# Optimization experiments

Hardware: AMD Instinct MI355X
Metric: run time of the kernel (lower is better)

The kernel has to match this reference:

```python
import jax, jax.numpy as jnp
import numpy as np

D_MODEL, D_FF, N_EXPERTS, TOP_K = 1024, 2048, 8, 2
B, S = 2, 2048

def setup_inputs() -> dict:
    key = jax.random.key(0)
    k1, k2, k3, k4 = jax.random.split(key, 4)
    scale = 0.02
    return {
        "x": jax.random.normal(k1, (B, S, D_MODEL), dtype=jnp.float32),
        "gate_w": jax.random.normal(k2, (D_MODEL, N_EXPERTS), dtype=jnp.float32) * scale,
        "w1": jax.random.normal(k3, (N_EXPERTS, D_MODEL, D_FF), dtype=jnp.float32) * scale,
        "w2": jax.random.normal(k4, (N_EXPERTS, D_FF, D_MODEL), dtype=jnp.float32) * scale,
    }

def reference(x, gate_w, w1, w2):
    # --- Router (eval mode: no exploration noise, no dropout) ---
    router_logits = jnp.einsum('bsd,de->bse', x, gate_w)          # [B,S,E]
    top_logits, top_idx = jax.lax.top_k(router_logits, TOP_K)      # [B,S,K]
    top_w = jax.nn.softmax(top_logits, axis=-1)                    # [B,S,K]
    # topk indices are distinct per token, so per-(token,expert) combine weight
    # is the sum over k of weight_k * 1[idx_k == e] (matches torch gather/argmax logic)
    combine = jnp.sum(
        jax.nn.one_hot(top_idx, N_EXPERTS, dtype=x.dtype) * top_w[..., None],
        axis=-2)                                                   # [B,S,E]
    # --- Experts: dense-compute formulation of the gather/MLP/scatter loop ---
    h = jax.nn.silu(jnp.einsum('bsd,edf->ebsf', x, w1))            # [E,B,S,Dff]
    y = jnp.einsum('ebsf,efd->ebsd', h, w2)                        # [E,B,S,D]
    out = jnp.einsum('ebsd,bse->bsd', y, combine)                  # [B,S,D]
    return out
```

## Files before the change

### kernel.cpp

```cpp
#include <hip/hip_runtime.h>
#include <cstdint>
#include <cstddef>

#define D_MODEL 1024
#define D_FF    2048
#define N_EXP   8
#define NTOK    4096
#define NASSIGN (NTOK * 2)
#define MAXTILE 72

typedef __bf16 bf16_t;
typedef bf16_t bf16x8 __attribute__((ext_vector_type(8)));
typedef float  f32x4  __attribute__((ext_vector_type(4)));

typedef __attribute__((address_space(3))) void       lds_void;
typedef const __attribute__((address_space(1))) void gl_void;

__device__ __forceinline__ unsigned short f2b(float f) {
  union { float f; unsigned u; } v; v.f = f;
  unsigned u = v.u;
  unsigned r = (u + 0x7FFFu + ((u >> 16) & 1u)) >> 16;
  return (unsigned short)r;
}
__device__ __forceinline__ float b2f(unsigned short b) {
  union { unsigned u; float f; } v; v.u = ((unsigned)b) << 16; return v.f;
}

__device__ __forceinline__ void transpose_strip4(
    const float* __restrict__ ein, unsigned short* __restrict__ eout,
    int R, int C, int c00, int r0, unsigned* T0, unsigned* T1, int tid)
{
  const int g = tid >> 4;
  const int m = tid & 15;
  const int sh = (g & 1) * 16;

  float4 v[4][4];
  #pragma unroll
  for (int t = 0; t < 4; ++t)
    #pragma unroll
    for (int i = 0; i < 4; ++i)
      v[t][i] = *(const float4*)(ein + (size_t)(r0 + i * 16 + g) * C + (c00 + t * 64) + m * 4);

  #define PACK(BUF, VT)                                                      \
    _Pragma("unroll")                                                        \
    for (int i = 0; i < 4; ++i) {                                            \
      unsigned lo = (unsigned)f2b(VT[i].x) | ((unsigned)f2b(VT[i].y) << 16); \
      unsigned hi = (unsigned)f2b(VT[i].z) | ((unsigned)f2b(VT[i].w) << 16); \
      unsigned* p = (BUF) + (i * 16 + g) * 33 + m * 2;                       \
      p[0] = lo; p[1] = hi;                                                  \
    }
  #define STORE(BUF, T)                                                      \
    _Pragma("unroll")                                                        \
    for (int i = 0; i < 4; ++i) {                                            \
      int c = i * 16 + g;                                                    \
      ushort4 o;                                                             \
      o.x = (unsigned short)((BUF)[(4 * m + 0) * 33 + (c >> 1)] >> sh);      \
      o.y = (unsigned short)((BUF)[(4 * m + 1) * 33 + (c >> 1)] >> sh);      \
      o.z = (unsigned short)((BUF)[(4 * m + 2) * 33 + (c >> 1)] >> sh);      \
      o.w = (unsigned short)((BUF)[(4 * m + 3) * 33 + (c >> 1)] >> sh);      \
      *(ushort4*)(eout + (size_t)(c00 + (T) * 64 + c) * R + r0 + m * 4) = o; \
    }

  PACK(T0, v[0]);
  __syncthreads();
  STORE(T0, 0); PACK(T1, v[1]);
  __syncthreads();
  STORE(T1, 1); PACK(T0, v[2]);
  __syncthreads();
  STORE(T0, 2); PACK(T1, v[3]);
  __syncthreads();
  STORE(T1, 3);
  #undef PACK
  #undef STORE
}

__global__ __launch_bounds__(256) void prep_k(
    const float* __restrict__ x, const float* __restrict__ gw,
    const float* __restrict__ w1, const float* __restrict__ w2,
    unsigned short* __restrict__ w1t, unsigned short* __restrict__ w2t,
    int* __restrict__ eidx, float* __restrict__ ewt)
{
  __shared__ unsigned T[2][64 * 33];
  const int bid = blockIdx.x;
  const int tid = threadIdx.x;

  if (bid < 1024) {
    int e = bid >> 7, rem = bid & 127;
    int bs = rem & 7, by = rem >> 3;
    transpose_strip4(w1 + (size_t)e * D_MODEL * D_FF,
                     w1t + (size_t)e * D_MODEL * D_FF,
                     D_MODEL, D_FF, bs * 256, by * 64, T[0], T[1], tid);
    return;
  }
  if (bid < 2048) {
    int b = bid - 1024;
    int e = b >> 7, rem = b & 127;
    int bs = rem & 3, by = rem >> 2;
    transpose_strip4(w2 + (size_t)e * D_MODEL * D_FF,
                     w2t + (size_t)e * D_MODEL * D_FF,
                     D_FF, D_MODEL, bs * 256, by * 64, T[0], T[1], tid);
    return;
  }
  const int rb = bid - 2048;
  const int wv = tid >> 6, lane = tid & 63;
  const int token = rb * 4 + wv;
  const float4* xr4 = (const float4*)(x + (size_t)token * D_MODEL);
  const float4* gw4 = (const float4*)gw;

  float acc[8] = {};
  #pragma unroll
  for (int it = 0; it < 4; ++it) {
    float4 xv = xr4[it * 64 + lane];
    int d0 = it * 256 + lane * 4;
    #pragma unroll
    for (int i = 0; i < 4; ++i) {
      int d = d0 + i;
      float4 g0 = gw4[d * 2];
      float4 g1 = gw4[d * 2 + 1];
      float xs = (i == 0) ? xv.x : (i == 1) ? xv.y : (i == 2) ? xv.z : xv.w;
      acc[0] += xs * g0.x; acc[1] += xs * g0.y;
      acc[2] += xs * g0.z; acc[3] += xs * g0.w;
      acc[4] += xs * g1.x; acc[5] += xs * g1.y;
      acc[6] += xs * g1.z; acc[7] += xs * g1.w;
    }
  }
  #pragma unroll
  for (int m = 1; m < 64; m <<= 1) {
    #pragma unroll
    for (int k = 0; k < 8; ++k) acc[k] += __shfl_xor(acc[k], m);
  }
  if (lane == 0) {
    int i1 = 0; float v1 = acc[0];
    #pragma unroll
    for (int k = 1; k < 8; ++k) if (acc[k] > v1) { v1 = acc[k]; i1 = k; }
    int i2 = -1; float v2 = -1e30f;
    #pragma unroll
    for (int k = 0; k < 8; ++k) if (k != i1 && acc[k] > v2) { v2 = acc[k]; i2 = k; }
    float t  = __expf(v2 - v1);
    float wa = 1.f / (1.f + t);
    float wb = t * wa;
    eidx[token * 2 + 0] = i1; eidx[token * 2 + 1] = i2;
    ewt [token * 2 + 0] = wa; ewt [token * 2 + 1] = wb;
  }
}

__global__ __launch_bounds__(1024) void scan_k(
    const int* __restrict__ eidx, const float* __restrict__ ewt,
    int* __restrict__ counts, int* __restrict__ offsets,
    int* __restrict__ rowtok, float* __restrict__ rowwt, int* __restrict__ rowof,
    int* __restrict__ tile_e, int* __restrict__ tile_m0, int* __restrict__ tile_n)
{
  __shared__ int wtot[16][9];
  __shared__ int woff[16][9];
  __shared__ int soff[8];
  const int t = threadIdx.x, w = t >> 6, lane = t & 63;

  int4 a = ((const int4*)eidx)[t * 2];
  int4 b = ((const int4*)eidx)[t * 2 + 1];
  int my[8] = {a.x, a.y, a.z, a.w, b.x, b.y, b.z, b.w};
  int pre[8], local[8] = {};
  #pragma unroll
  for (int i = 0; i < 8; ++i) { pre[i] = local[my[i]]; local[my[i]]++; }

  int inc[8];
  #pragma unroll
  for (int e = 0; e < 8; ++e) inc[e] = local[e];
  #pragma unroll
  for (int d = 1; d < 64; d <<= 1) {
    #pragma unroll
    for (int e = 0; e < 8; ++e) {
      int v = __shfl_up(inc[e], d);
      if (lane >= d) inc[e] += v;
    }
  }
  if (lane == 63) {
    #pragma unroll
    for (int e = 0; e < 8; ++e) wtot[w][e] = inc[e];
  }
  __syncthreads();

  if (t < 8) {
    int e = t, run = 0;
    #pragma unroll
    for (int ww = 0; ww < 16; ++ww) { woff[ww][e] = run; run += wtot[ww][e]; }
    wtot[0][e] = run;
  }
  __syncthreads();

  if (t == 0) {
    int o = 0, tt = 0;
    for (int e = 0; e < 8; ++e) {
      int c = wtot[0][e];
      counts[e] = c;
      offsets[e] = o;
      soff[e] = o;
      int nt = (c + 127) >> 7;
      for (int i = 0; i < nt; ++i) { tile_e[tt] = e; tile_m0[tt] = i * 128; ++tt; }
      o += c;
    }
    tile_n[0] = tt;
  }
  __syncthreads();

  int base_[8];
  #pragma unroll
  for (int e = 0; e < 8; ++e) base_[e] = soff[e] + woff[w][e] + inc[e] - local[e];

  float4 wa4 = ((const float4*)ewt)[t * 2];
  float4 wb4 = ((const float4*)ewt)[t * 2 + 1];
  float wv[8] = {wa4.x, wa4.y, wa4.z, wa4.w, wb4.x, wb4.y, wb4.z, wb4.w};

  #pragma unroll
  for (int i = 0; i < 8; ++i) {
    int bb = t * 8 + i, e = my[i];
    int row = base_[e] + pre[i];
    rowtok[row] = bb >> 1;
    rowwt[row]  = wv[i];
    rowof[bb]   = row;
  }
}

__global__ __launch_bounds__(256) void gather_k(
    const float* __restrict__ x, const int* __restrict__ rowtok,
    unsigned short* __restrict__ Xe)
{
  const int row = blockIdx.x;
  const int token = rowtok[row];
  const float4* xr = (const float4*)(x + (size_t)token * D_MODEL);
  ushort4* dst = (ushort4*)(Xe + (size_t)row * D_MODEL);
  float4 v = xr[threadIdx.x];
  ushort4 o;
  o.x = f2b(v.x); o.y = f2b(v.y); o.z = f2b(v.z); o.w = f2b(v.w);
  dst[threadIdx.x] = o;
}

template<int K, int N, int NT_LOG2, int MODE>
__global__ __launch_bounds__(256) void moe_gemm_k(
    const unsigned short* __restrict__ A,
    const unsigned short* __restrict__ Bt,
    unsigned short* __restrict__ Hout,
    const int* __restrict__ counts, const int* __restrict__ offsets,
    const float* __restrict__ rowwt,
    const int* __restrict__ tile_e, const int* __restrict__ tile_m0,
    const int* __restrict__ tile_n)
{
  const int nm = tile_n[0];
  const int nitems = nm << NT_LOG2;
  const int per = (nitems + 7) >> 3;
  const int w = (blockIdx.x & 7) * per + (blockIdx.x >> 3);
  if (w >= nitems) return;
  const int nidx = w / nm;
  const int t = w - nidx * nm;
  const int e   = tile_e[t];
  const int m0  = tile_m0[t];
  const int n0  = nidx * 128;
  const int cnt = counts[e];
  const int base = offsets[e];

  __shared__ unsigned short lA[128 * 32];
  __shared__ unsigned short lB[128 * 32];

  const int tid = threadIdx.x;
  const int lane = tid & 63;
  const int wv = tid >> 6;
  const int wm = wv & 1, wn = wv >> 1;
  const int col = lane & 15, quad = lane >> 4;

  const unsigned short* Aseg = A + (size_t)base * K;
  const unsigned short* Bseg = Bt + (size_t)e * ((size_t)N * K);

  const int lrow = lane >> 2;
  const int gch  = (lane & 3) ^ ((lane >> 2) & 3) ^ ((lane >> 4) & 3);
  const int fsw  = (col & 3) ^ ((col >> 2) & 3);

  f32x4 acc[4][4] = {};

  for (int k0 = 0; k0 < K; k0 += 32) {
    __syncthreads();
    #pragma unroll
    for (int r = 0; r < 2; ++r) {
      int s = r * 4 + wv;
      int row = s * 16 + lrow;
      const char* gA = (const char*)Aseg + ((size_t)(m0 + row) * K + k0) * 2 + gch * 16;
      const char* gB = (const char*)Bseg + ((size_t)(n0 + row) * K + k0) * 2 + gch * 16;
      __builtin_amdgcn_global_load_lds((gl_void*)gA, (lds_void*)((char*)lA + s * 1024), 16, 0, 0);
      __builtin_amdgcn_global_load_lds((gl_void*)gB, (lds_void*)((char*)lB + s * 1024), 16, 0, 0);
    }
    __syncthreads();

    bf16x8 af[4], bfr[4];
    #pragma unroll
    for (int i = 0; i < 4; ++i) {
      int r = wm * 64 + i * 16 + col;
      int p = quad ^ fsw;
      af[i] = *(const bf16x8*)(lA + r * 32 + p * 8);
    }
    #pragma unroll
    for (int j = 0; j < 4; ++j) {
      int r = wn * 64 + j * 16 + col;
      int p = quad ^ fsw;
      bfr[j] = *(const bf16x8*)(lB + r * 32 + p * 8);
    }
    #pragma unroll
    for (int i = 0; i < 4; ++i)
      #pragma unroll
      for (int j = 0; j < 4; ++j)
        acc[i][j] = __builtin_amdgcn_mfma_f32_16x16x32_bf16(af[i], bfr[j], acc[i][j], 0, 0, 0);
  }

  #pragma unroll
  for (int i = 0; i < 4; ++i) {
    #pragma unroll
    for (int reg = 0; reg < 4; ++reg) {
      int r = m0 + wm * 64 + i * 16 + quad * 4 + reg;
      if (r < cnt) {
        unsigned short* hrow = Hout + (size_t)(base + r) * N + (n0 + wn * 64 + col);
        if (MODE == 1) {
          #pragma unroll
          for (int j = 0; j < 4; ++j) {
            float v = acc[i][j][reg];
            float s = v / (1.f + __expf(-v));
            hrow[j * 16] = f2b(s);
          }
        } else {
          float wgt = rowwt[base + r];
          #pragma unroll
          for (int j = 0; j < 4; ++j)
            hrow[j * 16] = f2b(wgt * acc[i][j][reg]);
        }
      }
    }
  }
}

__global__ __launch_bounds__(256) void combine_k(
    const unsigned short* __restrict__ Y, const int* __restrict__ rowof,
    float* __restrict__ out)
{
  const int token = blockIdx.x;
  const int r1 = rowof[token * 2];
  const int r2 = rowof[token * 2 + 1];
  const int d4 = threadIdx.x;
  ushort4 a = *(const ushort4*)(Y + (size_t)r1 * D_MODEL + d4 * 4);
  ushort4 b = *(const ushort4*)(Y + (size_t)r2 * D_MODEL + d4 * 4);
  float4 o;
  o.x = b2f(a.x) + b2f(b.x);
  o.y = b2f(a.y) + b2f(b.y);
  o.z = b2f(a.z) + b2f(b.z);
  o.w = b2f(a.w) + b2f(b.w);
  *(float4*)(out + (size_t)token * D_MODEL + d4 * 4) = o;
}

extern "C" void kernel_launch(void* const* d_in, const int* in_sizes, int n_in,
                              void* d_out, int out_size, void* d_ws, size_t ws_size,
                              hipStream_t stream) {
  const float* x  = (const float*)d_in[0];
  const float* gw = (const float*)d_in[1];
  const float* w1 = (const float*)d_in[2];
  const float* w2 = (const float*)d_in[3];
  float* out = (float*)d_out;

  char* ws = (char*)d_ws;
  size_t off = 0;
  auto alloc = [&](size_t bytes) -> char* {
    char* p = ws + off; off += (bytes + 255) & ~(size_t)255; return p;
  };
  int*   ctrl    = (int*)alloc(1024);
  int*   counts  = ctrl;
  int*   offsets = ctrl + 8;
  int*   tile_n  = ctrl + 16;
  int*   tile_e  = ctrl + 32;
  int*   tile_m0 = ctrl + 32 + MAXTILE;
  int*   eidx    = (int*)  alloc((size_t)NASSIGN * 4);
  float* ewt     = (float*)alloc((size_t)NASSIGN * 4);
  int*   rowtok  = (int*)  alloc((size_t)NASSIGN * 4);
  float* rowwt   = (float*)alloc((size_t)NASSIGN * 4);
  int*   rowof   = (int*)  alloc((size_t)NASSIGN * 4);
  unsigned short* Xe  = (unsigned short*)alloc((size_t)(NASSIGN + 128) * D_MODEL * 2);
  unsigned short* H   = (unsigned short*)alloc((size_t)(NASSIGN + 128) * D_FF * 2);
  unsigned short* Y   = (unsigned short*)alloc((size_t)(NASSIGN + 128) * D_MODEL * 2);
  unsigned short* w1t = (unsigned short*)alloc((size_t)N_EXP * D_MODEL * D_FF * 2);
  unsigned short* w2t = (unsigned short*)alloc((size_t)N_EXP * D_MODEL * D_FF * 2);

  prep_k<<<2048 + NTOK / 4, 256, 0, stream>>>(x, gw, w1, w2, w1t, w2t, eidx, ewt);
  scan_k<<<1, 1024, 0, stream>>>(eidx, ewt, counts, offsets, rowtok, rowwt, rowof,
                                 tile_e, tile_m0, tile_n);
  gather_k<<<NASSIGN, 256, 0, stream>>>(x, rowtok, Xe);

  moe_gemm_k<D_MODEL, D_FF, 4, 1><<<MAXTILE * 16, 256, 0, stream>>>(
      Xe, w1t, H, counts, offsets, rowwt, tile_e, tile_m0, tile_n);
  moe_gemm_k<D_FF, D_MODEL, 3, 2><<<MAXTILE * 8, 256, 0, stream>>>(
      H, w2t, Y, counts, offsets, rowwt, tile_e, tile_m0, tile_n);
  combine_k<<<NTOK, 256, 0, stream>>>(Y, rowof, out);
}
```

Before: 351.0 us.

## Split-K the second expert GEMM and sum partials in combine

The down-projection GEMM now splits its K dimension in two across blockIdx.y, and each half writes a separate bf16 partial Y buffer. The combine kernel then sums both partials for both expert assignments of each token. The block-to-work mapping is also simplified from a strided XCD-aware interleave to a direct tile-major index. The aim is more blocks to fill CUs in the K=2048 GEMM, at the cost of extra Y write and read traffic, an extra bf16 rounding of partial sums, and possible loss of L2 locality from dropping the interleave.

New measurement: 348.4 us. About the same (-0.7%).

```diff
diff --git a/kernel.cpp b/kernel.cpp
--- a/kernel.cpp
+++ b/kernel.cpp
@@ -8,6 +8,7 @@
 #define NTOK    4096
 #define NASSIGN (NTOK * 2)
 #define MAXTILE 72
+#define YROWS   (NASSIGN + 128)
 
 typedef __bf16 bf16_t;
 typedef bf16_t bf16x8 __attribute__((ext_vector_type(8)));
@@ -234,7 +235,7 @@
   dst[threadIdx.x] = o;
 }
 
-template<int K, int N, int NT_LOG2, int MODE>
+template<int K, int N, int NT_LOG2, int MODE, int SPLITK>
 __global__ __launch_bounds__(256) void moe_gemm_k(
     const unsigned short* __restrict__ A,
     const unsigned short* __restrict__ Bt,
@@ -244,18 +245,17 @@
     const int* __restrict__ tile_e, const int* __restrict__ tile_m0,
     const int* __restrict__ tile_n)
 {
-  const int nm = tile_n[0];
-  const int nitems = nm << NT_LOG2;
-  const int per = (nitems + 7) >> 3;
-  const int w = (blockIdx.x & 7) * per + (blockIdx.x >> 3);
-  if (w >= nitems) return;
-  const int nidx = w / nm;
-  const int t = w - nidx * nm;
+  const int t = blockIdx.x >> NT_LOG2;
+  if (t >= tile_n[0]) return;
   const int e   = tile_e[t];
   const int m0  = tile_m0[t];
-  const int n0  = nidx * 128;
+  const int n0  = (blockIdx.x & ((1 << NT_LOG2) - 1)) * 128;
   const int cnt = counts[e];
   const int base = offsets[e];
+  const int ks   = blockIdx.y;
+  const int kbeg = ks * (K / SPLITK);
+  const int kend = kbeg + (K / SPLITK);
+  unsigned short* __restrict__ Hs = Hout + (size_t)ks * ((size_t)YROWS * N);
 
   __shared__ unsigned short lA[128 * 32];
   __shared__ unsigned short lB[128 * 32];
@@ -275,7 +275,7 @@
 
   f32x4 acc[4][4] = {};
 
-  for (int k0 = 0; k0 < K; k0 += 32) {
+  for (int k0 = kbeg; k0 < kend; k0 += 32) {
     __syncthreads();
     #pragma unroll
     for (int r = 0; r < 2; ++r) {
@@ -314,7 +314,7 @@
     for (int reg = 0; reg < 4; ++reg) {
       int r = m0 + wm * 64 + i * 16 + quad * 4 + reg;
       if (r < cnt) {
-        unsigned short* hrow = Hout + (size_t)(base + r) * N + (n0 + wn * 64 + col);
+        unsigned short* hrow = Hs + (size_t)(base + r) * N + (n0 + wn * 64 + col);
         if (MODE == 1) {
           #pragma unroll
           for (int j = 0; j < 4; ++j) {
@@ -341,13 +341,16 @@
   const int r1 = rowof[token * 2];
   const int r2 = rowof[token * 2 + 1];
   const int d4 = threadIdx.x;
-  ushort4 a = *(const ushort4*)(Y + (size_t)r1 * D_MODEL + d4 * 4);
-  ushort4 b = *(const ushort4*)(Y + (size_t)r2 * D_MODEL + d4 * 4);
+  const unsigned short* Y1 = Y + (size_t)YROWS * D_MODEL;
+  ushort4 a0 = *(const ushort4*)(Y  + (size_t)r1 * D_MODEL + d4 * 4);
+  ushort4 a1 = *(const ushort4*)(Y1 + (size_t)r1 * D_MODEL + d4 * 4);
+  ushort4 b0 = *(const ushort4*)(Y  + (size_t)r2 * D_MODEL + d4 * 4);
+  ushort4 b1 = *(const ushort4*)(Y1 + (size_t)r2 * D_MODEL + d4 * 4);
   float4 o;
-  o.x = b2f(a.x) + b2f(b.x);
-  o.y = b2f(a.y) + b2f(b.y);
-  o.z = b2f(a.z) + b2f(b.z);
-  o.w = b2f(a.w) + b2f(b.w);
+  o.x = (b2f(a0.x) + b2f(a1.x)) + (b2f(b0.x) + b2f(b1.x));
+  o.y = (b2f(a0.y) + b2f(a1.y)) + (b2f(b0.y) + b2f(b1.y));
+  o.z = (b2f(a0.z) + b2f(a1.z)) + (b2f(b0.z) + b2f(b1.z));
+  o.w = (b2f(a0.w) + b2f(a1.w)) + (b2f(b0.w) + b2f(b1.w));
   *(float4*)(out + (size_t)token * D_MODEL + d4 * 4) = o;
 }
 
@@ -376,9 +379,9 @@
   int*   rowtok  = (int*)  alloc((size_t)NASSIGN * 4);
   float* rowwt   = (float*)alloc((size_t)NASSIGN * 4);
   int*   rowof   = (int*)  alloc((size_t)NASSIGN * 4);
-  unsigned short* Xe  = (unsigned short*)alloc((size_t)(NASSIGN + 128) * D_MODEL * 2);
-  unsigned short* H   = (unsigned short*)alloc((size_t)(NASSIGN + 128) * D_FF * 2);
-  unsigned short* Y   = (unsigned short*)alloc((size_t)(NASSIGN + 128) * D_MODEL * 2);
+  unsigned short* Xe  = (unsigned short*)alloc((size_t)YROWS * D_MODEL * 2);
+  unsigned short* H   = (unsigned short*)alloc((size_t)YROWS * D_FF * 2);
+  unsigned short* Y   = (unsigned short*)alloc((size_t)YROWS * D_MODEL * 2 * 2);
   unsigned short* w1t = (unsigned short*)alloc((size_t)N_EXP * D_MODEL * D_FF * 2);
   unsigned short* w2t = (unsigned short*)alloc((size_t)N_EXP * D_MODEL * D_FF * 2);
 
@@ -387,9 +390,9 @@
                                  tile_e, tile_m0, tile_n);
   gather_k<<<NASSIGN, 256, 0, stream>>>(x, rowtok, Xe);
 
-  moe_gemm_k<D_MODEL, D_FF, 4, 1><<<MAXTILE * 16, 256, 0, stream>>>(
+  moe_gemm_k<D_MODEL, D_FF, 4, 1, 1><<<dim3(MAXTILE * 16, 1), 256, 0, stream>>>(
       Xe, w1t, H, counts, offsets, rowwt, tile_e, tile_m0, tile_n);
-  moe_gemm_k<D_FF, D_MODEL, 3, 2><<<MAXTILE * 8, 256, 0, stream>>>(
+  moe_gemm_k<D_FF, D_MODEL, 3, 2, 2><<<dim3(MAXTILE * 8, 2), 256, 0, stream>>>(
       H, w2t, Y, counts, offsets, rowwt, tile_e, tile_m0, tile_n);
   combine_k<<<NTOK, 256, 0, stream>>>(Y, rowof, out);
 }
```
